# Optimization experiments

Hardware: AMD Instinct MI355X
Metric: run time of the kernel (lower is better)

## Reference

```python
import jax, jax.numpy as jnp
import numpy as np

N1 = 64          # n1 (rows of matching matrix)
N2 = 64          # n2 (cols); N = n1*n2 association-graph nodes
N = N1 * N2
DENSITY = 0.15   # sparsity of affinity matrix K
CH = [64, 64, 64]
TAU = 0.05
SK_ITERS = 20


def _sinkhorn(s):
    # log-domain Sinkhorn, tau=0.05, 20 alternating row/col normalizations.
    # n1 == n2 here, so the dummy_row padding in the original is a no-op.
    log_s = s / TAU
    for i in range(SK_ITERS):
        log_s = log_s - jax.nn.logsumexp(log_s, axis=(1 if i % 2 == 0 else 0), keepdims=True)
    return jnp.exp(log_s)


def _lin(k, i, o, scale=0.1):
    kw, kb = jax.random.split(k)
    return (jax.random.normal(kw, (i, o), jnp.float32) * scale,
            jax.random.normal(kb, (o,), jnp.float32) * scale)


def setup_inputs() -> dict:
    key = jax.random.key(0)
    ks = jax.random.split(key, 16)
    mask = jax.random.uniform(ks[0], (N, N)) < DENSITY
    mask = mask | jnp.eye(N, dtype=bool)          # diag(K) supplies node features
    K = jnp.where(mask, jax.random.normal(ks[1], (N, N), jnp.float32), 0.0)
    # identical to torch: (K != 0).nonzero(as_tuple=False).t()
    edge_index = jnp.stack(jnp.nonzero(K)).astype(jnp.int32)
    inp = {"K": K, "edge_index": edge_index, "n1": N1, "n2": N2}
    dims_in = [1, CH[0], CH[1]]
    ki = 2
    for l in range(3):
        cw, cb = _lin(ks[ki], dims_in[l], CH[l]); ki += 1
        sw, sb = _lin(ks[ki], dims_in[l], CH[l]); ki += 1
        kw, kb = _lin(ks[ki], CH[l], 1); ki += 1
        inp.update({f"conv_w{l}": cw, f"conv_b{l}": cb,
                    f"self_w{l}": sw, f"self_b{l}": sb,
                    f"cls_w{l}": kw, f"cls_b{l}": kb})
    fw, fb = _lin(ks[ki], CH[2], 1)
    inp["fin_w"] = fw
    inp["fin_b"] = fb
    return inp


def _forward(K, edge_index, n1, n2, layer_params, fin_w, fin_b):
    n_nodes = n1 * n2
    src, dst = edge_index[0], edge_index[1]
    loop = jnp.arange(n_nodes, dtype=src.dtype)
    # PyG gcn_norm / add_remaining_self_loops: existing self-loop edges get
    # weight replaced (zeroed here, re-added with weight 1 below).
    w = jnp.concatenate([(src != dst).astype(K.dtype), jnp.ones((n_nodes,), K.dtype)])
    src_f = jnp.concatenate([src, loop])
    dst_f = jnp.concatenate([dst, loop])
    deg = jax.ops.segment_sum(w, dst_f, num_segments=n_nodes)
    dis = jnp.where(deg > 0, jax.lax.rsqrt(deg), 0.0)
    norm = dis[src_f] * w * dis[dst_f]                    # (E+N,)

    x = jnp.diag(K)[:, None]                              # (N, 1) node features
    for (cw, cb, sw, sb, kw, kb) in layer_params:
        xw = x @ cw                                       # (N, out)
        x_neigh = jax.ops.segment_sum(norm[:, None] * xw[src_f], dst_f,
                                      num_segments=n_nodes) + cb
        x_out = (x @ sw + sb) + x_neigh                   # self-loop + GCNConv
        sk = _sinkhorn((x_out @ kw + kb).reshape(n1, n2))
        x = x_out + sk.reshape(n_nodes, 1)                # broadcast over channels
    scores = x @ fin_w + fin_b                            # (N, 1)
    s = scores.reshape(n2, n1).T                          # (n1, n2)
    return _sinkhorn(s)


def reference(K, edge_index, n1, n2,
              conv_w0, conv_b0, self_w0, self_b0, cls_w0, cls_b0,
              conv_w1, conv_b1, self_w1, self_b1, cls_w1, cls_b1,
              conv_w2, conv_b2, self_w2, self_b2, cls_w2, cls_b2,
              fin_w, fin_b):
    layer_params = [(conv_w0, conv_b0, self_w0, self_b0, cls_w0, cls_b0),
                    (conv_w1, conv_b1, self_w1, self_b1, cls_w1, cls_b1),
                    (conv_w2, conv_b2, self_w2, self_b2, cls_w2, cls_b2)]
    return _forward(K, edge_index, n1, n2, layer_params, fin_w, fin_b)
```

## Files before the change

kernel.cpp:

```cpp
#include <hip/hip_runtime.h>
#include <hip/hip_bf16.h>
#include <cstdint>
#include <cstddef>

#define NN 4096

typedef float f32x4 __attribute__((ext_vector_type(4)));
typedef short s16x8 __attribute__((ext_vector_type(8)));

__global__ __launch_bounds__(256) void k_prep(const float* __restrict__ K,
    unsigned* __restrict__ degc, unsigned long long* __restrict__ maskT) {
  const int lane = threadIdx.x & 63;
  const int wv = threadIdx.x >> 6;
  const int d0 = blockIdx.x * 256 + lane * 4;
  const int sbase = blockIdx.y * 256 + wv * 64;
  const int chunk = blockIdx.y * 4 + wv;
  unsigned long long w0 = 0, w1 = 0, w2 = 0, w3 = 0;
#pragma unroll 8
  for (int i = 0; i < 64; ++i) {
    const float4 kv = *(const float4*)(K + (size_t)(sbase + i) * NN + d0);
    w0 |= ((unsigned long long)(kv.x != 0.0f)) << i;
    w1 |= ((unsigned long long)(kv.y != 0.0f)) << i;
    w2 |= ((unsigned long long)(kv.z != 0.0f)) << i;
    w3 |= ((unsigned long long)(kv.w != 0.0f)) << i;
  }
  unsigned long long* mp = maskT + (size_t)chunk * NN + d0;
  mp[0] = w0; mp[1] = w1; mp[2] = w2; mp[3] = w3;
  atomicAdd(&degc[d0 + 0], (unsigned)__popcll(w0));
  atomicAdd(&degc[d0 + 1], (unsigned)__popcll(w1));
  atomicAdd(&degc[d0 + 2], (unsigned)__popcll(w2));
  atomicAdd(&degc[d0 + 3], (unsigned)__popcll(w3));
}

__device__ __forceinline__ void sinkhorn_wave(float (&m)[64], float* lds, int lane) {
  for (int it = 0; it < 20; ++it) {
    float a0 = m[0], a1 = m[1], a2 = m[2], a3 = m[3];
#pragma unroll
    for (int j = 4; j < 64; j += 4) {
      a0 = fmaxf(a0, m[j]);     a1 = fmaxf(a1, m[j + 1]);
      a2 = fmaxf(a2, m[j + 2]); a3 = fmaxf(a3, m[j + 3]);
    }
    const float mx = fmaxf(fmaxf(a0, a1), fmaxf(a2, a3));
    float s0 = 0.f, s1 = 0.f, s2 = 0.f, s3 = 0.f;
#pragma unroll
    for (int j = 0; j < 64; j += 4) {
      s0 += __expf(m[j] - mx);     s1 += __expf(m[j + 1] - mx);
      s2 += __expf(m[j + 2] - mx); s3 += __expf(m[j + 3] - mx);
    }
    const float lse = mx + __logf((s0 + s1) + (s2 + s3));
#pragma unroll
    for (int j = 0; j < 64; ++j) m[j] -= lse;
    if (it < 19) {
#pragma unroll
      for (int j = 0; j < 64; ++j) lds[lane * 65 + j] = m[j];
      asm volatile("s_waitcnt lgkmcnt(0)" ::: "memory");
#pragma unroll
      for (int j = 0; j < 64; ++j) m[j] = lds[j * 65 + lane];
      asm volatile("" ::: "memory");
    }
  }
#pragma unroll
  for (int j = 0; j < 64; ++j) lds[j * 65 + lane] = m[j];
  asm volatile("s_waitcnt lgkmcnt(0)" ::: "memory");
}

__global__ __launch_bounds__(256) void k_xform0(const float* __restrict__ K,
    const unsigned* __restrict__ degc,
    const float* __restrict__ cw, const float* __restrict__ cb,
    const float* __restrict__ sw, const float* __restrict__ sb,
    __hip_bfloat16* __restrict__ gHi, __hip_bfloat16* __restrict__ gLo,
    float* __restrict__ xselfT) {
  const int lane = threadIdx.x & 63;
  const int wv = threadIdx.x >> 6;
  const int s = blockIdx.x * 64 + lane;
  const float xv = K[(size_t)s * NN + s];
  const float ds = rsqrtf((float)degc[s]);
#pragma unroll
  for (int i = 0; i < 16; ++i) {
    const int c = wv * 16 + i;
    const float gv = ds * xv * cw[c];
    const __hip_bfloat16 hi = __float2bfloat16(gv);
    gHi[(size_t)c * NN + s] = hi;
    gLo[(size_t)c * NN + s] = __float2bfloat16(gv - __bfloat162float(hi));
    xselfT[(size_t)c * NN + s] = xv * sw[c] + sb[c] + cb[c];
  }
}

__global__ __launch_bounds__(256, 1) void k_xform(const float* __restrict__ vT,
    const float* __restrict__ xoutT, const unsigned* __restrict__ degc,
    const float* __restrict__ cw, const float* __restrict__ cb,
    const float* __restrict__ sw, const float* __restrict__ sb,
    __hip_bfloat16* __restrict__ gHi, __hip_bfloat16* __restrict__ gLo,
    float* __restrict__ xselfT) {
  __shared__ float skl[64 * 65];
  __shared__ float xt[64][64];
  __shared__ float wcl[64 * 32], wsl[64 * 32];
  const int tid = threadIdx.x;
  const int lane = tid & 63;
  const int wv = tid >> 6;
  const int s = blockIdx.x * 64 + lane;
  const int cbase = blockIdx.y * 32;
  if (wv == 0) {
    float m[64];
#pragma unroll
    for (int j = 0; j < 64; ++j) m[j] = vT[j * 64 + lane] * 20.0f;
    sinkhorn_wave(m, skl, lane);
  } else if (wv == 1) {
#pragma unroll
    for (int k = 0; k < 32; ++k) xt[k][lane] = xoutT[(size_t)k * NN + s];
  } else if (wv == 2) {
#pragma unroll
    for (int k = 32; k < 64; ++k) xt[k][lane] = xoutT[(size_t)k * NN + s];
  } else {
#pragma unroll
    for (int q = 0; q < 32; ++q) {
      const int e = q * 64 + lane;
      wcl[e] = cw[(e >> 5) * 64 + cbase + (e & 31)];
      wsl[e] = sw[(e >> 5) * 64 + cbase + (e & 31)];
    }
  }
  __syncthreads();
  const float skv = __expf(skl[blockIdx.x * 65 + lane]);
#pragma unroll
  for (int i = 0; i < 16; ++i) xt[wv * 16 + i][lane] += skv;
  __syncthreads();
  float accC[8], accS[8];
#pragma unroll
  for (int i = 0; i < 8; ++i) { accC[i] = 0.f; accS[i] = 0.f; }
  for (int k = 0; k < 64; ++k) {
    const float xv = xt[k][lane];
#pragma unroll
    for (int i = 0; i < 8; ++i) {
      accC[i] = fmaf(xv, wcl[k * 32 + wv * 8 + i], accC[i]);
      accS[i] = fmaf(xv, wsl[k * 32 + wv * 8 + i], accS[i]);
    }
  }
  const float ds = rsqrtf((float)degc[s]);
#pragma unroll
  for (int i = 0; i < 8; ++i) {
    const int c = cbase + wv * 8 + i;
    const float gv = ds * accC[i];
    const __hip_bfloat16 hi = __float2bfloat16(gv);
    gHi[(size_t)c * NN + s] = hi;
    gLo[(size_t)c * NN + s] = __float2bfloat16(gv - __bfloat162float(hi));
    xselfT[(size_t)c * NN + s] = accS[i] + sb[c] + cb[c];
  }
}

__global__ __launch_bounds__(512) void k_agg(const unsigned long long* __restrict__ maskT,
    const __hip_bfloat16* __restrict__ gHi, const __hip_bfloat16* __restrict__ gLo,
    const float* __restrict__ xselfT, const unsigned* __restrict__ degc,
    const float* __restrict__ kw, const float* __restrict__ kb,
    float* __restrict__ xoutT, float* __restrict__ vT) {
  const int tid = threadIdx.x;
  const int lane = tid & 63;
  const int wv = tid >> 6;
  const int mtile = wv & 3;
  const int ks = wv >> 2;
  const int l15 = lane & 15;
  const int h = lane >> 4;
  const int d = blockIdx.x * 16 + l15;
  const int ch = mtile * 16 + l15;
  const short* __restrict__ gh = (const short*)gHi;
  const short* __restrict__ gl = (const short*)gLo;
  f32x4 acch = {0.f, 0.f, 0.f, 0.f};
  f32x4 accl = {0.f, 0.f, 0.f, 0.f};
  const int c0 = ks * 32;
#pragma unroll 4
  for (int c = c0; c < c0 + 32; ++c) {
    const unsigned long long w = maskT[(size_t)c * NN + d];
    const unsigned half0 = (unsigned)w, half1 = (unsigned)(w >> 32);
#pragma unroll
    for (int t = 0; t < 2; ++t) {
      const unsigned half = t ? half1 : half0;
      const unsigned hb = (half >> (8 * h)) & 0xFFu;
      s16x8 bfr;
#pragma unroll
      for (int j = 0; j < 8; ++j)
        bfr[j] = (short)(((hb >> j) & 1u) * 0x3F80u);
      const size_t abase = (size_t)ch * NN + (size_t)(c * 64 + t * 32 + 8 * h);
      const s16x8 ah = *(const s16x8*)(gh + abase);
      const s16x8 al = *(const s16x8*)(gl + abase);
      acch = __builtin_amdgcn_mfma_f32_16x16x32_bf16(ah, bfr, acch, 0, 0, 0);
      accl = __builtin_amdgcn_mfma_f32_16x16x32_bf16(al, bfr, accl, 0, 0, 0);
    }
  }
  __shared__ float rbuf[4][64][5];
  __shared__ float vred[16][17];
  f32x4 tot;
#pragma unroll
  for (int r = 0; r < 4; ++r) tot[r] = acch[r] + accl[r];
  if (ks == 1) {
#pragma unroll
    for (int r = 0; r < 4; ++r) rbuf[mtile][lane][r] = tot[r];
  }
  __syncthreads();
  if (ks == 0) {
    const float dd = rsqrtf((float)degc[d]);
    float p = 0.f;
#pragma unroll
    for (int r = 0; r < 4; ++r) {
      const int chr = mtile * 16 + h * 4 + r;
      const float xo = xselfT[(size_t)chr * NN + d] + dd * (tot[r] + rbuf[mtile][lane][r]);
      xoutT[(size_t)chr * NN + d] = xo;
      p = fmaf(xo, kw[chr], p);
    }
    vred[l15][mtile * 4 + h] = p;
  }
  __syncthreads();
  if (tid < 16) {
    float sum = kb[0];
#pragma unroll
    for (int q = 0; q < 16; ++q) sum += vred[tid][q];
    const int d2 = blockIdx.x * 16 + tid;
    vT[(d2 & 63) * 64 + (d2 >> 6)] = sum;
  }
}

__global__ __launch_bounds__(256, 1) void k_scores(const float* __restrict__ vT,
    const float* __restrict__ xoutT, const float* __restrict__ fw,
    const float* __restrict__ fb, float* __restrict__ scores) {
  __shared__ float skl[64 * 65];
  __shared__ float fwl[64];
  const int tid = threadIdx.x;
  const int lane = tid & 63;
  const int wv = tid >> 6;
  if (wv == 0) {
    float m[64];
#pragma unroll
    for (int j = 0; j < 64; ++j) m[j] = vT[j * 64 + lane] * 20.0f;
    sinkhorn_wave(m, skl, lane);
  } else if (wv == 1) {
    fwl[lane] = fw[lane];
  }
  __syncthreads();
  const int n = blockIdx.x * 256 + tid;
  const float skv = __expf(skl[(n >> 6) * 65 + (n & 63)]);
  float acc = 0.f, sumw = 0.f;
#pragma unroll 8
  for (int k = 0; k < 64; ++k) {
    const float w = fwl[k];
    sumw += w;
    acc = fmaf(xoutT[(size_t)k * NN + n], w, acc);
  }
  scores[n] = acc + skv * sumw + fb[0];
}

__global__ __launch_bounds__(64, 1) void k_skfinal(const float* __restrict__ scores,
                                                   float* __restrict__ out) {
  __shared__ float lds[64 * 65];
  const int lane = threadIdx.x;
  float m[64];
#pragma unroll
  for (int j = 0; j < 64; ++j) m[j] = scores[j * 64 + lane] * 20.0f;
  sinkhorn_wave(m, lds, lane);
#pragma unroll
  for (int j = 0; j < 64; ++j) out[j * 64 + lane] = __expf(m[j]);
}

extern "C" void kernel_launch(void* const* d_in, const int* in_sizes, int n_in,
                              void* d_out, int out_size, void* d_ws, size_t ws_size,
                              hipStream_t stream) {
  const float* K = (const float*)d_in[0];
  const float* cw[3] = {(const float*)d_in[4],  (const float*)d_in[10], (const float*)d_in[16]};
  const float* cb[3] = {(const float*)d_in[5],  (const float*)d_in[11], (const float*)d_in[17]};
  const float* sw[3] = {(const float*)d_in[6],  (const float*)d_in[12], (const float*)d_in[18]};
  const float* sb[3] = {(const float*)d_in[7],  (const float*)d_in[13], (const float*)d_in[19]};
  const float* kw[3] = {(const float*)d_in[8],  (const float*)d_in[14], (const float*)d_in[20]};
  const float* kb[3] = {(const float*)d_in[9],  (const float*)d_in[15], (const float*)d_in[21]};
  const float* fw = (const float*)d_in[22];
  const float* fb = (const float*)d_in[23];
  float* out = (float*)d_out;

  char* ws = (char*)d_ws;
  const size_t KB = 1024, MB = 1024 * 1024;
  unsigned* degc            = (unsigned*)(ws + 0);
  float* vT                 = (float*)(ws + 32 * KB);
  float* scores             = (float*)(ws + 48 * KB);
  unsigned long long* maskT = (unsigned long long*)(ws + 64 * KB);
  __hip_bfloat16* gHi       = (__hip_bfloat16*)(ws + 64 * KB + 2 * MB);
  __hip_bfloat16* gLo       = (__hip_bfloat16*)(ws + 64 * KB + 2 * MB + 512 * KB);
  float* xselfT             = (float*)(ws + 64 * KB + 3 * MB);
  float* xoutT              = (float*)(ws + 64 * KB + 4 * MB);
  (void)in_sizes; (void)n_in; (void)out_size; (void)ws_size;

  hipMemsetAsync(degc, 0, NN * sizeof(unsigned), stream);
  k_prep<<<dim3(16, 16), 256, 0, stream>>>(K, degc, maskT);

  k_xform0<<<64, 256, 0, stream>>>(K, degc, cw[0], cb[0], sw[0], sb[0], gHi, gLo, xselfT);
  k_agg<<<256, 512, 0, stream>>>(maskT, gHi, gLo, xselfT, degc, kw[0], kb[0], xoutT, vT);
  for (int l = 1; l < 3; ++l) {
    k_xform<<<dim3(64, 2), 256, 0, stream>>>(vT, xoutT, degc, cw[l], cb[l], sw[l], sb[l],
                                             gHi, gLo, xselfT);
    k_agg<<<256, 512, 0, stream>>>(maskT, gHi, gLo, xselfT, degc, kw[l], kb[l], xoutT, vT);
  }
  k_scores<<<16, 256, 0, stream>>>(vT, xoutT, fw, fb, scores);
  k_skfinal<<<1, 64, 0, stream>>>(scores, out);
}
```

Baseline: 232.9 us.

## Use potential-form Sinkhorn, overlap it with the GEMM, fuse final kernels, drop atomics

Sinkhorn now tracks only row and column potentials U and V, so each iteration no longer rewrites the whole 64x64 matrix in LDS. In k_xform a dedicated extra wave runs Sinkhorn while the other four waves compute the per-node linear transforms; the Sinkhorn broadcast term is folded in afterwards through column sums of the weights (x+s)W = xW + s·sum(W). Degree counting moves from atomics plus a memset into k_xform0, which popcounts the mask and stores the inverse square root degree once. The scores and final Sinkhorn kernels are merged into one single-block kernel, which trades one launch for less parallelism in the score computation.

```diff
diff --git a/kernel.cpp b/kernel.cpp
--- a/kernel.cpp
+++ b/kernel.cpp
@@ -9,7 +9,7 @@
 typedef short s16x8 __attribute__((ext_vector_type(8)));
 
 __global__ __launch_bounds__(256) void k_prep(const float* __restrict__ K,
-    unsigned* __restrict__ degc, unsigned long long* __restrict__ maskT) {
+                                              unsigned long long* __restrict__ maskT) {
   const int lane = threadIdx.x & 63;
   const int wv = threadIdx.x >> 6;
   const int d0 = blockIdx.x * 256 + lane * 4;
@@ -26,55 +26,67 @@
   }
   unsigned long long* mp = maskT + (size_t)chunk * NN + d0;
   mp[0] = w0; mp[1] = w1; mp[2] = w2; mp[3] = w3;
-  atomicAdd(&degc[d0 + 0], (unsigned)__popcll(w0));
-  atomicAdd(&degc[d0 + 1], (unsigned)__popcll(w1));
-  atomicAdd(&degc[d0 + 2], (unsigned)__popcll(w2));
-  atomicAdd(&degc[d0 + 3], (unsigned)__popcll(w3));
-}
-
-__device__ __forceinline__ void sinkhorn_wave(float (&m)[64], float* lds, int lane) {
+}
+
+__device__ __forceinline__ void sinkhorn_pot(const float (&a)[64], float* __restrict__ mat,
+                                             float* __restrict__ p64, int lane) {
+  float U = 0.f, V = 0.f;
   for (int it = 0; it < 20; ++it) {
-    float a0 = m[0], a1 = m[1], a2 = m[2], a3 = m[3];
+    float t[64];
+    if ((it & 1) == 0) {
+      p64[lane] = V;
+      asm volatile("s_waitcnt lgkmcnt(0)" ::: "memory");
+#pragma unroll
+      for (int j = 0; j < 64; ++j) t[j] = a[j] - p64[j];
+    } else {
+      p64[lane] = U;
+      asm volatile("s_waitcnt lgkmcnt(0)" ::: "memory");
+#pragma unroll
+      for (int j = 0; j < 64; ++j) t[j] = mat[j * 65 + lane] - p64[j];
+    }
+    float m0 = t[0], m1 = t[1], m2 = t[2], m3 = t[3];
 #pragma unroll
     for (int j = 4; j < 64; j += 4) {
-      a0 = fmaxf(a0, m[j]);     a1 = fmaxf(a1, m[j + 1]);
-      a2 = fmaxf(a2, m[j + 2]); a3 = fmaxf(a3, m[j + 3]);
-    }
-    const float mx = fmaxf(fmaxf(a0, a1), fmaxf(a2, a3));
+      m0 = fmaxf(m0, t[j]);     m1 = fmaxf(m1, t[j + 1]);
+      m2 = fmaxf(m2, t[j + 2]); m3 = fmaxf(m3, t[j + 3]);
+    }
+    const float mx = fmaxf(fmaxf(m0, m1), fmaxf(m2, m3));
     float s0 = 0.f, s1 = 0.f, s2 = 0.f, s3 = 0.f;
 #pragma unroll
     for (int j = 0; j < 64; j += 4) {
-      s0 += __expf(m[j] - mx);     s1 += __expf(m[j + 1] - mx);
-      s2 += __expf(m[j + 2] - mx); s3 += __expf(m[j + 3] - mx);
+      s0 += __expf(t[j] - mx);     s1 += __expf(t[j + 1] - mx);
+      s2 += __expf(t[j + 2] - mx); s3 += __expf(t[j + 3] - mx);
     }
     const float lse = mx + __logf((s0 + s1) + (s2 + s3));
-#pragma unroll
-    for (int j = 0; j < 64; ++j) m[j] -= lse;
-    if (it < 19) {
-#pragma unroll
-      for (int j = 0; j < 64; ++j) lds[lane * 65 + j] = m[j];
-      asm volatile("s_waitcnt lgkmcnt(0)" ::: "memory");
-#pragma unroll
-      for (int j = 0; j < 64; ++j) m[j] = lds[j * 65 + lane];
-      asm volatile("" ::: "memory");
-    }
-  }
-#pragma unroll
-  for (int j = 0; j < 64; ++j) lds[j * 65 + lane] = m[j];
+    if ((it & 1) == 0) U = lse; else V = lse;
+  }
+  p64[lane] = V;
   asm volatile("s_waitcnt lgkmcnt(0)" ::: "memory");
+#pragma unroll
+  for (int j = 0; j < 64; ++j) mat[lane * 65 + j] = a[j] - U - p64[j];
+  asm volatile("s_waitcnt lgkmcnt(0)" ::: "memory");
 }
 
 __global__ __launch_bounds__(256) void k_xform0(const float* __restrict__ K,
-    const unsigned* __restrict__ degc,
+    const unsigned long long* __restrict__ maskT,
     const float* __restrict__ cw, const float* __restrict__ cb,
     const float* __restrict__ sw, const float* __restrict__ sb,
+    float* __restrict__ disv,
     __hip_bfloat16* __restrict__ gHi, __hip_bfloat16* __restrict__ gLo,
     float* __restrict__ xselfT) {
+  __shared__ float pdeg[4][64];
   const int lane = threadIdx.x & 63;
   const int wv = threadIdx.x >> 6;
   const int s = blockIdx.x * 64 + lane;
+  unsigned cnt = 0;
+#pragma unroll
+  for (int q = 0; q < 16; ++q)
+    cnt += (unsigned)__popcll(maskT[(size_t)(wv * 16 + q) * NN + s]);
+  pdeg[wv][lane] = (float)cnt;
+  __syncthreads();
+  const float ds = rsqrtf(pdeg[0][lane] + pdeg[1][lane] + pdeg[2][lane] + pdeg[3][lane]);
+  if (wv == 0) disv[s] = ds;
   const float xv = K[(size_t)s * NN + s];
-  const float ds = rsqrtf((float)degc[s]);
 #pragma unroll
   for (int i = 0; i < 16; ++i) {
     const int c = wv * 16 + i;
@@ -86,13 +98,14 @@
   }
 }
 
-__global__ __launch_bounds__(256, 1) void k_xform(const float* __restrict__ vT,
-    const float* __restrict__ xoutT, const unsigned* __restrict__ degc,
+__global__ __launch_bounds__(320, 1) void k_xform(const float* __restrict__ vT,
+    const float* __restrict__ xoutT, const float* __restrict__ disv,
     const float* __restrict__ cw, const float* __restrict__ cb,
     const float* __restrict__ sw, const float* __restrict__ sb,
     __hip_bfloat16* __restrict__ gHi, __hip_bfloat16* __restrict__ gLo,
     float* __restrict__ xselfT) {
   __shared__ float skl[64 * 65];
+  __shared__ float p64[64];
   __shared__ float xt[64][64];
   __shared__ float wcl[64 * 32], wsl[64 * 32];
   const int tid = threadIdx.x;
@@ -100,56 +113,65 @@
   const int wv = tid >> 6;
   const int s = blockIdx.x * 64 + lane;
   const int cbase = blockIdx.y * 32;
+  float a[64];
   if (wv == 0) {
-    float m[64];
-#pragma unroll
-    for (int j = 0; j < 64; ++j) m[j] = vT[j * 64 + lane] * 20.0f;
-    sinkhorn_wave(m, skl, lane);
-  } else if (wv == 1) {
-#pragma unroll
-    for (int k = 0; k < 32; ++k) xt[k][lane] = xoutT[(size_t)k * NN + s];
-  } else if (wv == 2) {
-#pragma unroll
-    for (int k = 32; k < 64; ++k) xt[k][lane] = xoutT[(size_t)k * NN + s];
+#pragma unroll
+    for (int j = 0; j < 64; ++j) {
+      a[j] = vT[j * 64 + lane] * 20.0f;
+      skl[lane * 65 + j] = a[j];
+    }
   } else {
-#pragma unroll
-    for (int q = 0; q < 32; ++q) {
-      const int e = q * 64 + lane;
-      wcl[e] = cw[(e >> 5) * 64 + cbase + (e & 31)];
-      wsl[e] = sw[(e >> 5) * 64 + cbase + (e & 31)];
-    }
-  }
-  __syncthreads();
-  const float skv = __expf(skl[blockIdx.x * 65 + lane]);
-#pragma unroll
-  for (int i = 0; i < 16; ++i) xt[wv * 16 + i][lane] += skv;
-  __syncthreads();
-  float accC[8], accS[8];
-#pragma unroll
-  for (int i = 0; i < 8; ++i) { accC[i] = 0.f; accS[i] = 0.f; }
-  for (int k = 0; k < 64; ++k) {
-    const float xv = xt[k][lane];
+    const int w = wv - 1;
+#pragma unroll
+    for (int r = 0; r < 16; ++r)
+      xt[w * 16 + r][lane] = xoutT[(size_t)(w * 16 + r) * NN + s];
+#pragma unroll
+    for (int q = 0; q < 8; ++q) {
+      const int e = w * 512 + q * 64 + lane;
+      const int k = e >> 5, cl = e & 31;
+      wcl[e] = cw[k * 64 + cbase + cl];
+      wsl[e] = sw[k * 64 + cbase + cl];
+    }
+  }
+  __syncthreads();
+  float accC[8], accS[8], csum[8], ssum[8];
+  if (wv == 0) {
+    sinkhorn_pot(a, skl, p64, lane);
+  } else {
+    const int cl0 = (wv - 1) * 8;
+#pragma unroll
+    for (int i = 0; i < 8; ++i) { accC[i] = 0.f; accS[i] = 0.f; csum[i] = 0.f; ssum[i] = 0.f; }
+    for (int k = 0; k < 64; ++k) {
+      const float xv = xt[k][lane];
+#pragma unroll
+      for (int i = 0; i < 8; ++i) {
+        const float wc = wcl[k * 32 + cl0 + i];
+        const float ws_ = wsl[k * 32 + cl0 + i];
+        accC[i] = fmaf(xv, wc, accC[i]);  csum[i] += wc;
+        accS[i] = fmaf(xv, ws_, accS[i]); ssum[i] += ws_;
+      }
+    }
+  }
+  __syncthreads();
+  if (wv > 0) {
+    const float skv = __expf(skl[blockIdx.x * 65 + lane]);
+    const float ds = disv[s];
+    const int cl0 = (wv - 1) * 8;
 #pragma unroll
     for (int i = 0; i < 8; ++i) {
-      accC[i] = fmaf(xv, wcl[k * 32 + wv * 8 + i], accC[i]);
-      accS[i] = fmaf(xv, wsl[k * 32 + wv * 8 + i], accS[i]);
-    }
-  }
-  const float ds = rsqrtf((float)degc[s]);
-#pragma unroll
-  for (int i = 0; i < 8; ++i) {
-    const int c = cbase + wv * 8 + i;
-    const float gv = ds * accC[i];
-    const __hip_bfloat16 hi = __float2bfloat16(gv);
-    gHi[(size_t)c * NN + s] = hi;
-    gLo[(size_t)c * NN + s] = __float2bfloat16(gv - __bfloat162float(hi));
-    xselfT[(size_t)c * NN + s] = accS[i] + sb[c] + cb[c];
+      const int c = cbase + cl0 + i;
+      const float gv = ds * (accC[i] + skv * csum[i]);
+      const __hip_bfloat16 hi = __float2bfloat16(gv);
+      gHi[(size_t)c * NN + s] = hi;
+      gLo[(size_t)c * NN + s] = __float2bfloat16(gv - __bfloat162float(hi));
+      xselfT[(size_t)c * NN + s] = accS[i] + skv * ssum[i] + sb[c] + cb[c];
+    }
   }
 }
 
 __global__ __launch_bounds__(512) void k_agg(const unsigned long long* __restrict__ maskT,
     const __hip_bfloat16* __restrict__ gHi, const __hip_bfloat16* __restrict__ gLo,
-    const float* __restrict__ xselfT, const unsigned* __restrict__ degc,
+    const float* __restrict__ xselfT, const float* __restrict__ disv,
     const float* __restrict__ kw, const float* __restrict__ kb,
     float* __restrict__ xoutT, float* __restrict__ vT) {
   const int tid = threadIdx.x;
@@ -196,7 +218,7 @@
   }
   __syncthreads();
   if (ks == 0) {
-    const float dd = rsqrtf((float)degc[d]);
+    const float dd = disv[d];
     float p = 0.f;
 #pragma unroll
     for (int r = 0; r < 4; ++r) {
@@ -217,45 +239,57 @@
   }
 }
 
-__global__ __launch_bounds__(256, 1) void k_scores(const float* __restrict__ vT,
+__global__ __launch_bounds__(512, 1) void k_final(const float* __restrict__ vT,
     const float* __restrict__ xoutT, const float* __restrict__ fw,
-    const float* __restrict__ fb, float* __restrict__ scores) {
+    const float* __restrict__ fb, float* __restrict__ out) {
   __shared__ float skl[64 * 65];
-  __shared__ float fwl[64];
+  __shared__ float scp[64 * 65];
+  __shared__ float p64[64];
+  __shared__ float sumw_sh;
   const int tid = threadIdx.x;
   const int lane = tid & 63;
   const int wv = tid >> 6;
+  float a[64];
   if (wv == 0) {
-    float m[64];
-#pragma unroll
-    for (int j = 0; j < 64; ++j) m[j] = vT[j * 64 + lane] * 20.0f;
-    sinkhorn_wave(m, skl, lane);
-  } else if (wv == 1) {
-    fwl[lane] = fw[lane];
-  }
-  __syncthreads();
-  const int n = blockIdx.x * 256 + tid;
-  const float skv = __expf(skl[(n >> 6) * 65 + (n & 63)]);
-  float acc = 0.f, sumw = 0.f;
+#pragma unroll
+    for (int j = 0; j < 64; ++j) {
+      a[j] = vT[j * 64 + lane] * 20.0f;
+      skl[lane * 65 + j] = a[j];
+    }
+    sinkhorn_pot(a, skl, p64, lane);
+  } else {
+    const float fbv = fb[0];
+    float sumw = 0.f;
+#pragma unroll
+    for (int k = 0; k < 64; ++k) sumw += fw[k];
+    for (int n = (wv - 1) * 64 + lane; n < NN; n += 448) {
+      float acc = fbv;
 #pragma unroll 8
-  for (int k = 0; k < 64; ++k) {
-    const float w = fwl[k];
-    sumw += w;
-    acc = fmaf(xoutT[(size_t)k * NN + n], w, acc);
-  }
-  scores[n] = acc + skv * sumw + fb[0];
-}
-
-__global__ __launch_bounds__(64, 1) void k_skfinal(const float* __restrict__ scores,
-                                                   float* __restrict__ out) {
-  __shared__ float lds[64 * 65];
-  const int lane = threadIdx.x;
-  float m[64];
-#pragma unroll
-  for (int j = 0; j < 64; ++j) m[j] = scores[j * 64 + lane] * 20.0f;
-  sinkhorn_wave(m, lds, lane);
-#pragma unroll
-  for (int j = 0; j < 64; ++j) out[j * 64 + lane] = __expf(m[j]);
+      for (int k = 0; k < 64; ++k) acc = fmaf(xoutT[(size_t)k * NN + n], fw[k], acc);
+      scp[(n & 63) * 65 + (n >> 6)] = acc;
+    }
+    if (tid == 64) sumw_sh = sumw;
+  }
+  __syncthreads();
+  const float sumw = sumw_sh;
+  for (int n = tid; n < NN; n += 512) {
+    const float sk2 = __expf(skl[(n >> 6) * 65 + (n & 63)]);
+    const int slot = (n & 63) * 65 + (n >> 6);
+    scp[slot] = (scp[slot] + sk2 * sumw) * 20.0f;
+  }
+  __syncthreads();
+  if (wv == 0) {
+    float a2[64];
+#pragma unroll
+    for (int j = 0; j < 64; ++j) a2[j] = scp[lane * 65 + j];
+    sinkhorn_pot(a2, scp, p64, lane);
+  }
+  __syncthreads();
+#pragma unroll
+  for (int q = 0; q < 8; ++q) {
+    const int e = q * 512 + tid;
+    out[e] = __expf(scp[(e >> 6) * 65 + (e & 63)]);
+  }
 }
 
 extern "C" void kernel_launch(void* const* d_in, const int* in_sizes, int n_in,
@@ -274,9 +308,8 @@
 
   char* ws = (char*)d_ws;
   const size_t KB = 1024, MB = 1024 * 1024;
-  unsigned* degc            = (unsigned*)(ws + 0);
+  float* disv               = (float*)(ws + 0);
   float* vT                 = (float*)(ws + 32 * KB);
-  float* scores             = (float*)(ws + 48 * KB);
   unsigned long long* maskT = (unsigned long long*)(ws + 64 * KB);
   __hip_bfloat16* gHi       = (__hip_bfloat16*)(ws + 64 * KB + 2 * MB);
   __hip_bfloat16* gLo       = (__hip_bfloat16*)(ws + 64 * KB + 2 * MB + 512 * KB);
@@ -284,16 +317,14 @@
   float* xoutT              = (float*)(ws + 64 * KB + 4 * MB);
   (void)in_sizes; (void)n_in; (void)out_size; (void)ws_size;
 
-  hipMemsetAsync(degc, 0, NN * sizeof(unsigned), stream);
-  k_prep<<<dim3(16, 16), 256, 0, stream>>>(K, degc, maskT);
-
-  k_xform0<<<64, 256, 0, stream>>>(K, degc, cw[0], cb[0], sw[0], sb[0], gHi, gLo, xselfT);
-  k_agg<<<256, 512, 0, stream>>>(maskT, gHi, gLo, xselfT, degc, kw[0], kb[0], xoutT, vT);
+  k_prep<<<dim3(16, 16), 256, 0, stream>>>(K, maskT);
+  k_xform0<<<64, 256, 0, stream>>>(K, maskT, cw[0], cb[0], sw[0], sb[0],
+                                   disv, gHi, gLo, xselfT);
+  k_agg<<<256, 512, 0, stream>>>(maskT, gHi, gLo, xselfT, disv, kw[0], kb[0], xoutT, vT);
   for (int l = 1; l < 3; ++l) {
-    k_xform<<<dim3(64, 2), 256, 0, stream>>>(vT, xoutT, degc, cw[l], cb[l], sw[l], sb[l],
+    k_xform<<<dim3(64, 2), 320, 0, stream>>>(vT, xoutT, disv, cw[l], cb[l], sw[l], sb[l],
                                              gHi, gLo, xselfT);
-    k_agg<<<256, 512, 0, stream>>>(maskT, gHi, gLo, xselfT, degc, kw[l], kb[l], xoutT, vT);
-  }
-  k_scores<<<16, 256, 0, stream>>>(vT, xoutT, fw, fb, scores);
-  k_skfinal<<<1, 64, 0, stream>>>(scores, out);
-}
+    k_agg<<<256, 512, 0, stream>>>(maskT, gHi, gLo, xselfT, disv, kw[l], kb[l], xoutT, vT);
+  }
+  k_final<<<1, 512, 0, stream>>>(vT, xoutT, fw, fb, out);
+}
```

Result: no change. 237.1 us (+1.8%).
